# Optimization experiments

Hardware: AMD Instinct MI355X
Metric: run time of the kernel (lower is better)

The kernel has to match this reference:

```python
import jax, jax.numpy as jnp
import numpy as np

N, E, D, H, C, ED = 50000, 800000, 128, 2, 128, 8
LEAKY_SLOPE = 0.2
SOFTMAX_EPS = 1e-16
LN_EPS = 1e-5


def setup_inputs() -> dict:
    key = jax.random.key(0)
    ks = jax.random.split(key, 12)
    s = lambda k, shp, scale: jax.random.normal(k, shp, dtype=jnp.float32) * scale
    return {
        "x": s(ks[0], (N, D), 1.0),
        "edge_index": jax.random.randint(ks[1], (2, E), 0, N, dtype=jnp.int64),
        "edge_attr": s(ks[2], (E, ED), 1.0),
        "W_ep": s(ks[3], (ED, D), 1.0 / np.sqrt(ED)),
        "b_ep": jnp.zeros((D,), jnp.float32),
        "W_lin": s(ks[4], (D, H * C), 1.0 / np.sqrt(D)),
        "att_src": s(ks[5], (H, C), 1.0 / np.sqrt(C)),
        "att_dst": s(ks[6], (H, C), 1.0 / np.sqrt(C)),
        "W_le": s(ks[7], (D, H * C), 1.0 / np.sqrt(D)),
        "att_edge": s(ks[8], (H, C), 1.0 / np.sqrt(C)),
        "bias_gat": jnp.zeros((C,), jnp.float32),
        "ln_gamma": jnp.ones((C,), jnp.float32),
        "ln_beta": jnp.zeros((C,), jnp.float32),
    }


def reference(x, edge_index, edge_attr, W_ep, b_ep, W_lin, att_src, att_dst,
              W_le, att_edge, bias_gat, ln_gamma, ln_beta):
    src, dst = edge_index[0], edge_index[1]
    # edge_proj: [E, ED] -> [E, D]
    e = edge_attr @ W_ep + b_ep
    # node projection: [N, H, C]
    h = (x @ W_lin).reshape(N, H, C)
    # edge projection inside GATConv: [E, H, C]
    ee = (e @ W_le).reshape(E, H, C)
    # attention logits
    a_src = jnp.einsum('nhc,hc->nh', h, att_src)      # [N, H]
    a_dst = jnp.einsum('nhc,hc->nh', h, att_dst)      # [N, H]
    a_edge = jnp.einsum('ehc,hc->eh', ee, att_edge)   # [E, H]
    score = a_src[src] + a_dst[dst] + a_edge          # [E, H]
    score = jnp.where(score >= 0, score, LEAKY_SLOPE * score)
    # segment softmax over incoming edges of each dst node
    smax = jax.ops.segment_max(score, dst, num_segments=N)     # [N, H]
    ex = jnp.exp(score - smax[dst])
    denom = jax.ops.segment_sum(ex, dst, num_segments=N)       # [N, H]
    alpha = ex / (denom[dst] + SOFTMAX_EPS)                    # [E, H]
    # message + scatter-add aggregation
    msg = h[src] * alpha[:, :, None]                           # [E, H, C]
    agg = jax.ops.segment_sum(msg, dst, num_segments=N)        # [N, H, C]
    out = agg.mean(axis=1) + bias_gat                          # concat=False -> head mean
    # residual + LayerNorm (dropout = identity in eval mode)
    y = out + x
    mu = y.mean(axis=-1, keepdims=True)
    var = y.var(axis=-1, keepdims=True)
    return (y - mu) * jax.lax.rsqrt(var + LN_EPS) * ln_gamma + ln_beta
```

## Files before the change

kernel.cpp:

```cpp
#include <hip/hip_runtime.h>
#include <hip/hip_bf16.h>

#define NN 50000
#define EE 800000
#define DD 128
#define HH 2
#define CC 128
#define HC 256
#define EDD 8

#define LEAKY 0.2f
#define SMEPS 1e-16f
#define LNEPS 1e-5f

#define SCAN_B 196
#define CONV_B 3125
#define K2_B   782
#define NPAD   50176

#define HB_OFF    0u
#define ASRC_OFF  12800000u
#define ADST_OFF  13200000u
#define CONST_OFF 13600000u
#define SD_OFF    13604096u
#define CNT8_OFF  20004096u
#define ROW_OFF   21609728u
#define BASE8_OFF 21810432u
#define PAY_OFF   23416064u
#define WBT_OFF   29816064u
#define BSUM_OFF  29881600u

typedef __attribute__((ext_vector_type(8))) short short8v;
typedef __attribute__((ext_vector_type(4))) float float4v;
typedef __attribute__((ext_vector_type(2))) int int2v;

__device__ __forceinline__ float bf2f(unsigned short v) {
  return __uint_as_float(((unsigned)v) << 16);
}
__device__ __forceinline__ unsigned short f2bf(float f) {
  __hip_bfloat16 b = __float2bfloat16(f);
  return *reinterpret_cast<unsigned short*>(&b);
}

__global__ __launch_bounds__(256) void kA_prep_convert(const float* __restrict__ W_lin,
                                                       const float* __restrict__ att_src,
                                                       const float* __restrict__ att_dst,
                                                       const float* __restrict__ W_le,
                                                       const float* __restrict__ att_edge,
                                                       const float* __restrict__ W_ep,
                                                       const float* __restrict__ b_ep,
                                                       const int* __restrict__ ei_raw,
                                                       float* __restrict__ consts,
                                                       unsigned short* __restrict__ wbT,
                                                       int* __restrict__ cnt8,
                                                       int2v* __restrict__ sd) {
  int b = blockIdx.x, tid = threadIdx.x;
  if (b == 0) {
    __shared__ float vlds[HH * DD];
    int h = tid >> 7, d = tid & 127;
    const float* as = att_src + h * CC;
    const float* ad = att_dst + h * CC;
    const float* ae = att_edge + h * CC;
    float us = 0.f, ud = 0.f, vv = 0.f;
    for (int c = 0; c < CC; ++c) {
      float wl = W_lin[d * HC + h * CC + c];
      float we = W_le[d * HC + h * CC + c];
      us += wl * as[c]; ud += wl * ad[c]; vv += we * ae[c];
    }
    consts[h * 128 + d] = us;
    consts[256 + h * 128 + d] = ud;
    vlds[h * 128 + d] = vv;
    __syncthreads();
    if (tid < 16) {
      int hh = tid >> 3, k = tid & 7;
      float w = 0.f;
      for (int dd2 = 0; dd2 < DD; ++dd2) w += W_ep[k * DD + dd2] * vlds[hh * 128 + dd2];
      consts[512 + hh * 8 + k] = w;
    }
    if (tid < 2) {
      float ce = 0.f;
      for (int dd2 = 0; dd2 < DD; ++dd2) ce += b_ep[dd2] * vlds[tid * 128 + dd2];
      consts[528 + tid] = ce;
    }
  } else if (b <= 128) {
    int i = (b - 1) * 256 + tid;
    int k = i >> 8, c = i & 255;
    wbT[c * DD + k] = f2bf(W_lin[i]);
  } else {
    int lane = threadIdx.x & 63;
    int probe = ei_raw[2 * lane + 1];
    bool is64 = (__ballot(probe != 0) == 0ull);
    int xcd = __builtin_amdgcn_s_getreg((20) | (0 << 6) | ((32 - 1) << 11)) & 7;
    int i = (b - 129) * 256 + tid;
    int s, d;
    if (is64) { s = ei_raw[2 * i]; d = ei_raw[2 * (EE + i)]; }
    else      { s = ei_raw[i];     d = ei_raw[EE + i]; }
    int rk = __hip_atomic_fetch_add(&cnt8[xcd * NPAD + d], 1,
                                    __ATOMIC_RELAXED, __HIP_MEMORY_SCOPE_WORKGROUP);
    int2v v; v.x = s; v.y = d | (rk << 16) | (xcd << 29);
    sd[i] = v;
  }
}

__global__ __launch_bounds__(256) void k_scan1(const int* __restrict__ cnt8,
                                               int* __restrict__ rowstart,
                                               int* __restrict__ base8,
                                               int* __restrict__ bsum) {
  __shared__ int sp[256];
  int t = threadIdx.x, b = blockIdx.x;
  int n = b * 256 + t;
  int c[8];
  int tot = 0;
#pragma unroll
  for (int r = 0; r < 8; ++r) {
    c[r] = (n < NN) ? cnt8[r * NPAD + n] : 0;
    tot += c[r];
  }
  sp[t] = tot;
  __syncthreads();
  for (int off = 1; off < 256; off <<= 1) {
    int u = (t >= off) ? sp[t - off] : 0;
    __syncthreads();
    sp[t] += u;
    __syncthreads();
  }
  int intra = sp[t] - tot;
  if (n < NN) {
    rowstart[n] = intra;
    int run = intra;
#pragma unroll
    for (int r = 0; r < 8; ++r) { base8[r * NPAD + n] = run; run += c[r]; }
  }
  if (t == 255) bsum[b] = sp[255];
}

__global__ __launch_bounds__(256) void kB_scan_mfma(int* __restrict__ rowstart,
                                                    const int* __restrict__ bsum,
                                                    int* __restrict__ base8,
                                                    const float* __restrict__ x,
                                                    const unsigned short* __restrict__ wbT,
                                                    const float* __restrict__ consts,
                                                    unsigned char* __restrict__ hbuf8,
                                                    float* __restrict__ a_src,
                                                    float* __restrict__ a_dst) {
  __shared__ unsigned short xs[64 * 256];
  int tid = threadIdx.x;

  if (blockIdx.x < SCAN_B) {
    int* sp = (int*)xs;
    int t = tid, b = blockIdx.x;
    int v = (t < SCAN_B) ? bsum[t] : 0;
    sp[t] = v;
    __syncthreads();
    for (int off = 1; off < 256; off <<= 1) {
      int u = (t >= off) ? sp[t - off] : 0;
      __syncthreads();
      sp[t] += u;
      __syncthreads();
    }
    int boff = (b == 0) ? 0 : sp[b - 1];
    int n = b * 256 + t;
    if (n < NN) {
      rowstart[n] += boff;
#pragma unroll
      for (int r = 0; r < 8; ++r) base8[r * NPAD + n] += boff;
    }
    if (n == NN) rowstart[NN] = EE;
    return;
  }

  int n0 = (blockIdx.x - SCAN_B) * 64;
  int r = tid >> 2, q = tid & 3;
  int n = n0 + r;
  bool valid = (n < NN);

  float xv[32];
  const float4* xp = (const float4*)(x + (size_t)n * DD + q * 32);
#pragma unroll
  for (int j = 0; j < 8; ++j) {
    float4 v = valid ? xp[j] : make_float4(0.f, 0.f, 0.f, 0.f);
    xv[j * 4 + 0] = v.x; xv[j * 4 + 1] = v.y; xv[j * 4 + 2] = v.z; xv[j * 4 + 3] = v.w;
  }
  float ps0 = 0.f, ps1 = 0.f, pd0 = 0.f, pd1 = 0.f;
#pragma unroll
  for (int j = 0; j < 32; j += 4) {
    float4 u0 = *(const float4*)(consts +   0 + q * 32 + j);
    float4 u1 = *(const float4*)(consts + 128 + q * 32 + j);
    float4 v0 = *(const float4*)(consts + 256 + q * 32 + j);
    float4 v1 = *(const float4*)(consts + 384 + q * 32 + j);
    ps0 += xv[j] * u0.x + xv[j+1] * u0.y + xv[j+2] * u0.z + xv[j+3] * u0.w;
    ps1 += xv[j] * u1.x + xv[j+1] * u1.y + xv[j+2] * u1.z + xv[j+3] * u1.w;
    pd0 += xv[j] * v0.x + xv[j+1] * v0.y + xv[j+2] * v0.z + xv[j+3] * v0.w;
    pd1 += xv[j] * v1.x + xv[j+1] * v1.y + xv[j+2] * v1.z + xv[j+3] * v1.w;
  }
#pragma unroll
  for (int off = 1; off < 4; off <<= 1) {
    ps0 += __shfl_xor(ps0, off); ps1 += __shfl_xor(ps1, off);
    pd0 += __shfl_xor(pd0, off); pd1 += __shfl_xor(pd1, off);
  }
  if (q == 0 && valid) {
    *(float2*)(a_src + n * 2) = make_float2(ps0, ps1);
    *(float2*)(a_dst + n * 2) = make_float2(pd0, pd1);
  }

#pragma unroll
  for (int ci = 0; ci < 4; ++ci) {
    union { short8v v; unsigned short u[8]; } pk;
#pragma unroll
    for (int j = 0; j < 8; ++j) pk.u[j] = f2bf(xv[ci * 8 + j]);
    unsigned byte = r * 256 + (q * 4 + ci) * 16;
    byte ^= (r & 7) << 4;
    *(short8v*)((char*)xs + byte) = pk.v;
  }

  int wave = tid >> 6, l = tid & 63;
  int wc = wave * 64;
  int lr = l & 15, lg = l >> 4;
  short8v bfr[4][4];
#pragma unroll
  for (int ct = 0; ct < 4; ++ct) {
    int col = wc + ct * 16 + lr;
#pragma unroll
    for (int kt = 0; kt < 4; ++kt)
      bfr[ct][kt] = *(const short8v*)(wbT + (size_t)col * DD + kt * 32 + lg * 8);
  }

  __syncthreads();

  float4v acc[4][4];
#pragma unroll
  for (int rt = 0; rt < 4; ++rt)
#pragma unroll
    for (int ct = 0; ct < 4; ++ct) acc[rt][ct] = (float4v){0.f, 0.f, 0.f, 0.f};

#pragma unroll
  for (int kt = 0; kt < 4; ++kt) {
    short8v afr[4];
#pragma unroll
    for (int rt = 0; rt < 4; ++rt) {
      int row = rt * 16 + lr;
      unsigned byte = row * 256 + kt * 64 + lg * 16;
      byte ^= (row & 7) << 4;
      afr[rt] = *(const short8v*)((const char*)xs + byte);
    }
#pragma unroll
    for (int rt = 0; rt < 4; ++rt)
#pragma unroll
      for (int ct = 0; ct < 4; ++ct)
        acc[rt][ct] = __builtin_amdgcn_mfma_f32_16x16x32_bf16(afr[rt], bfr[ct][kt], acc[rt][ct], 0, 0, 0);
  }

  __syncthreads();
#pragma unroll
  for (int rt = 0; rt < 4; ++rt) {
#pragma unroll
    for (int j = 0; j < 4; ++j) {
      int row = rt * 16 + lg * 4 + j;
#pragma unroll
      for (int ct = 0; ct < 4; ++ct) {
        int col = wc + ct * 16 + lr;
        int idx2 = ((col & 127) << 1) | (col >> 7);
        unsigned o = (unsigned)idx2 * 2;
        unsigned byte = row * 512 + (o ^ ((((unsigned)(row & 7) ^ ((o >> 7) & 3))) << 4));
        *(unsigned short*)((char*)xs + byte) = f2bf(acc[rt][ct][j]);
      }
    }
  }
  __syncthreads();
  {
    int r2 = tid >> 2, q2 = tid & 3;
    int n2 = n0 + r2;
    if (n2 < NN) {
#pragma unroll
      for (int kk = 0; kk < 4; ++kk) {
        unsigned u4[4];
#pragma unroll
        for (int t2 = 0; t2 < 2; ++t2) {
          int k = kk * 2 + t2;
          unsigned o = q2 * 128 + k * 16;
          unsigned byte = r2 * 512 + (o ^ ((((unsigned)(r2 & 7) ^ ((o >> 7) & 3))) << 4));
          short8v v = *(short8v*)((char*)xs + byte);
          unsigned ua = __builtin_amdgcn_cvt_pk_fp8_f32(bf2f((unsigned short)v[0]), bf2f((unsigned short)v[1]), 0u, false);
          ua = __builtin_amdgcn_cvt_pk_fp8_f32(bf2f((unsigned short)v[2]), bf2f((unsigned short)v[3]), ua, true);
          unsigned ub = __builtin_amdgcn_cvt_pk_fp8_f32(bf2f((unsigned short)v[4]), bf2f((unsigned short)v[5]), 0u, false);
          ub = __builtin_amdgcn_cvt_pk_fp8_f32(bf2f((unsigned short)v[6]), bf2f((unsigned short)v[7]), ub, true);
          u4[t2 * 2] = ua; u4[t2 * 2 + 1] = ub;
        }
        uint4 w4 = make_uint4(u4[0], u4[1], u4[2], u4[3]);
        *(uint4*)(hbuf8 + (size_t)n2 * 256 + q2 * 64 + kk * 16) = w4;
      }
    }
  }
}

__global__ __launch_bounds__(256) void k34_edge(const int2v* __restrict__ sd,
                                                const int* __restrict__ base8,
                                                const float* __restrict__ edge_attr,
                                                const float* __restrict__ a_src,
                                                const float* __restrict__ a_dst,
                                                const float* __restrict__ consts,
                                                int2v* __restrict__ payload) {
  int e = blockIdx.x * 256 + threadIdx.x;
  int2v sdv = sd[e];
  int s = sdv.x;
  unsigned y = (unsigned)sdv.y;
  int d = (int)(y & 0xFFFFu);
  int rk = (int)((y >> 16) & 0x1FFFu);
  int xcd = (int)(y >> 29);
  float4 ea0 = *(const float4*)(edge_attr + (size_t)e * 8);
  float4 ea1 = *(const float4*)(edge_attr + (size_t)e * 8 + 4);
  float2 asv = *(const float2*)(a_src + s * 2);
  float2 adv = *(const float2*)(a_dst + d * 2);
  const float* w0 = consts + 512;
  const float* w1 = consts + 520;
  float sc0 = asv.x + adv.x + consts[528]
            + ea0.x * w0[0] + ea0.y * w0[1] + ea0.z * w0[2] + ea0.w * w0[3]
            + ea1.x * w0[4] + ea1.y * w0[5] + ea1.z * w0[6] + ea1.w * w0[7];
  float sc1 = asv.y + adv.y + consts[529]
            + ea0.x * w1[0] + ea0.y * w1[1] + ea0.z * w1[2] + ea0.w * w1[3]
            + ea1.x * w1[4] + ea1.y * w1[5] + ea1.z * w1[6] + ea1.w * w1[7];
  sc0 = (sc0 >= 0.f) ? sc0 : LEAKY * sc0;
  sc1 = (sc1 >= 0.f) ? sc1 : LEAKY * sc1;
  float ex0 = __expf(sc0);
  float ex1 = __expf(sc1);
  unsigned pk = (unsigned)f2bf(ex0) | ((unsigned)f2bf(ex1) << 16);
  int pos = base8[xcd * NPAD + d] + rk;
  int2v pv; pv.x = s << 8; pv.y = (int)pk;
  payload[pos] = pv;
}

__global__ __launch_bounds__(256) void k5_fused(const int* __restrict__ rowstart,
                                                const int2v* __restrict__ payload,
                                                const unsigned char* __restrict__ hb8,
                                                const float* __restrict__ x,
                                                const float* __restrict__ bias,
                                                const float* __restrict__ gamma,
                                                const float* __restrict__ beta,
                                                float* __restrict__ out) {
  int n = blockIdx.x * 4 + (threadIdx.x >> 6);
  int lane = threadIdx.x & 63;
  if (n >= NN) return;
  int p0i = __builtin_amdgcn_readfirstlane(rowstart[n]);
  int p1i = __builtin_amdgcn_readfirstlane(rowstart[n + 1]);
  int len = p1i - p0i;
  int c0 = lane * 2;
  const int2v* pp = payload + p0i;
  float a00 = 0.f, a01 = 0.f, a10 = 0.f, a11 = 0.f, se0 = 0.f, se1 = 0.f;

#define K5_LD(soff) (*(const unsigned*)(hb8 + (size_t)(unsigned)(soff) + lane * 4))
#define K5_ACC(pl, w) { \
    float ex0 = bf2f((unsigned short)((unsigned)(pl).y & 0xffffu)); \
    float ex1 = bf2f((unsigned short)(((unsigned)(pl).y) >> 16)); \
    a00 = fmaf(ex0, __builtin_amdgcn_cvt_f32_fp8((int)(w), 0), a00); \
    a01 = fmaf(ex1, __builtin_amdgcn_cvt_f32_fp8((int)(w), 1), a01); \
    a10 = fmaf(ex0, __builtin_amdgcn_cvt_f32_fp8((int)(w), 2), a10); \
    a11 = fmaf(ex1, __builtin_amdgcn_cvt_f32_fp8((int)(w), 3), a11); \
    se0 += ex0; se1 += ex1; }

  if (len > 0) {
    int2v p0 = pp[0];
    int2v p1 = (len > 1) ? pp[1] : p0;
    int2v p2 = (len > 2) ? pp[2] : p0;
    int2v p3 = (len > 3) ? pp[3] : p0;
    unsigned h0 = K5_LD(p0.x), h1 = K5_LD(p1.x), h2 = K5_LD(p2.x), h3 = K5_LD(p3.x);
    int i = 0;
    for (; i + 7 < len; i += 4) {
      int2v q0 = pp[i + 4], q1 = pp[i + 5], q2 = pp[i + 6], q3 = pp[i + 7];
      unsigned g0 = K5_LD(q0.x), g1 = K5_LD(q1.x), g2 = K5_LD(q2.x), g3 = K5_LD(q3.x);
      K5_ACC(p0, h0); K5_ACC(p1, h1); K5_ACC(p2, h2); K5_ACC(p3, h3);
      p0 = q0; p1 = q1; p2 = q2; p3 = q3;
      h0 = g0; h1 = g1; h2 = g2; h3 = g3;
    }
    int r = len - i;
    K5_ACC(p0, h0);
    if (r > 1) K5_ACC(p1, h1);
    if (r > 2) K5_ACC(p2, h2);
    if (r > 3) K5_ACC(p3, h3);
    if (r > 4) {
      int rem = r - 4;
      int2v q0 = pp[i + 4];
      int2v q1 = (rem > 1) ? pp[i + 5] : q0;
      int2v q2 = (rem > 2) ? pp[i + 6] : q0;
      unsigned g0 = K5_LD(q0.x), g1 = K5_LD(q1.x), g2 = K5_LD(q2.x);
      K5_ACC(q0, g0);
      if (rem > 1) K5_ACC(q1, g1);
      if (rem > 2) K5_ACC(q2, g2);
    }
  }
#undef K5_LD
#undef K5_ACC

  float inv0 = 0.5f / (se0 + SMEPS);
  float inv1 = 0.5f / (se1 + SMEPS);
  float2 xv = *(const float2*)(x + (size_t)n * DD + c0);
  float v0 = a00 * inv0 + a01 * inv1 + bias[c0] + xv.x;
  float v1 = a10 * inv0 + a11 * inv1 + bias[c0 + 1] + xv.y;
  float s = v0 + v1, ss = v0 * v0 + v1 * v1;
#pragma unroll
  for (int o = 32; o > 0; o >>= 1) {
    s += __shfl_xor(s, o);
    ss += __shfl_xor(ss, o);
  }
  float mu = s * (1.f / 128.f);
  float var = ss * (1.f / 128.f) - mu * mu;
  float rstd = rsqrtf(var + LNEPS);
  float2 ov;
  ov.x = (v0 - mu) * rstd * gamma[c0] + beta[c0];
  ov.y = (v1 - mu) * rstd * gamma[c0 + 1] + beta[c0 + 1];
  *(float2*)(out + (size_t)n * CC + c0) = ov;
}

extern "C" void kernel_launch(void* const* d_in, const int* in_sizes, int n_in,
                              void* d_out, int out_size, void* d_ws, size_t ws_size,
                              hipStream_t stream) {
  const float* x        = (const float*)d_in[0];
  const int*   ei_raw   = (const int*)d_in[1];
  const float* edge_attr= (const float*)d_in[2];
  const float* W_ep     = (const float*)d_in[3];
  const float* b_ep     = (const float*)d_in[4];
  const float* W_lin    = (const float*)d_in[5];
  const float* att_src  = (const float*)d_in[6];
  const float* att_dst  = (const float*)d_in[7];
  const float* W_le     = (const float*)d_in[8];
  const float* att_edge = (const float*)d_in[9];
  const float* bias_gat = (const float*)d_in[10];
  const float* ln_gamma = (const float*)d_in[11];
  const float* ln_beta  = (const float*)d_in[12];

  char* ws = (char*)d_ws;
  unsigned char* hbuf8 = (unsigned char*)(ws + HB_OFF);
  float*    a_src  = (float*)(ws + ASRC_OFF);
  float*    a_dst  = (float*)(ws + ADST_OFF);
  float*    consts = (float*)(ws + CONST_OFF);
  int2v*    sd     = (int2v*)(ws + SD_OFF);
  int*      cnt8   = (int*)(ws + CNT8_OFF);
  int*      rowst  = (int*)(ws + ROW_OFF);
  int*      base8  = (int*)(ws + BASE8_OFF);
  int2v*    payload= (int2v*)(ws + PAY_OFF);
  unsigned short* wbT = (unsigned short*)(ws + WBT_OFF);
  int*      bsum   = (int*)(ws + BSUM_OFF);

  hipMemsetAsync(cnt8, 0, (size_t)8 * NPAD * 4, stream);
  kA_prep_convert<<<129 + CONV_B, 256, 0, stream>>>(W_lin, att_src, att_dst, W_le, att_edge,
                                                    W_ep, b_ep, ei_raw, consts, wbT, cnt8, sd);
  k_scan1<<<SCAN_B, 256, 0, stream>>>(cnt8, rowst, base8, bsum);
  kB_scan_mfma<<<SCAN_B + K2_B, 256, 0, stream>>>(rowst, bsum, base8, x, wbT, consts, hbuf8, a_src, a_dst);
  k34_edge<<<CONV_B, 256, 0, stream>>>(sd, base8, edge_attr, a_src, a_dst, consts, payload);
  k5_fused<<<(NN + 3) / 4, 256, 0, stream>>>(rowst, payload, hbuf8, x, bias_gat, ln_gamma, ln_beta, (float*)d_out);
}
```

Baseline: 139.7 us.

## Restructure launch pipeline: fold memset, merge edge counting with GEMM, inline scan fixup

Replaces the hipMemsetAsync with zeroing inside the prep kernel. Moves the edge-counting atomics into the same launch as the MFMA node projection so the two overlap. Drops the separate second-level scan kernel: each block of the edge and aggregation kernels recomputes the 196-entry block-sum prefix in shared memory and adds it on the fly. This removes one memset and one kernel launch plus a pass over rowstart/base8, at the cost of a redundant small scan with many barriers in every block of two large kernels.

```diff
diff --git a/kernel.cpp b/kernel.cpp
--- a/kernel.cpp
+++ b/kernel.cpp
@@ -42,18 +42,16 @@
   return *reinterpret_cast<unsigned short*>(&b);
 }
 
-__global__ __launch_bounds__(256) void kA_prep_convert(const float* __restrict__ W_lin,
-                                                       const float* __restrict__ att_src,
-                                                       const float* __restrict__ att_dst,
-                                                       const float* __restrict__ W_le,
-                                                       const float* __restrict__ att_edge,
-                                                       const float* __restrict__ W_ep,
-                                                       const float* __restrict__ b_ep,
-                                                       const int* __restrict__ ei_raw,
-                                                       float* __restrict__ consts,
-                                                       unsigned short* __restrict__ wbT,
-                                                       int* __restrict__ cnt8,
-                                                       int2v* __restrict__ sd) {
+__global__ __launch_bounds__(256) void k1_prep(const float* __restrict__ W_lin,
+                                               const float* __restrict__ att_src,
+                                               const float* __restrict__ att_dst,
+                                               const float* __restrict__ W_le,
+                                               const float* __restrict__ att_edge,
+                                               const float* __restrict__ W_ep,
+                                               const float* __restrict__ b_ep,
+                                               float* __restrict__ consts,
+                                               unsigned short* __restrict__ wbT,
+                                               int* __restrict__ cnt8) {
   int b = blockIdx.x, tid = threadIdx.x;
   if (b == 0) {
     __shared__ float vlds[HH * DD];
@@ -87,11 +85,30 @@
     int k = i >> 8, c = i & 255;
     wbT[c * DD + k] = f2bf(W_lin[i]);
   } else {
-    int lane = threadIdx.x & 63;
+    int n = (b - 129) * 256 + tid;
+#pragma unroll
+    for (int r = 0; r < 8; ++r) cnt8[r * NPAD + n] = 0;
+  }
+}
+
+__global__ __launch_bounds__(256) void k2_conv_mfma(const float* __restrict__ x,
+                                                    const unsigned short* __restrict__ wbT,
+                                                    const float* __restrict__ consts,
+                                                    const int* __restrict__ ei_raw,
+                                                    unsigned char* __restrict__ hbuf8,
+                                                    float* __restrict__ a_src,
+                                                    float* __restrict__ a_dst,
+                                                    int* __restrict__ cnt8,
+                                                    int2v* __restrict__ sd) {
+  __shared__ unsigned short xs[64 * 256];
+  int tid = threadIdx.x;
+
+  if (blockIdx.x >= K2_B) {
+    int lane = tid & 63;
     int probe = ei_raw[2 * lane + 1];
     bool is64 = (__ballot(probe != 0) == 0ull);
     int xcd = __builtin_amdgcn_s_getreg((20) | (0 << 6) | ((32 - 1) << 11)) & 7;
-    int i = (b - 129) * 256 + tid;
+    int i = (blockIdx.x - K2_B) * 256 + tid;
     int s, d;
     if (is64) { s = ei_raw[2 * i]; d = ei_raw[2 * (EE + i)]; }
     else      { s = ei_raw[i];     d = ei_raw[EE + i]; }
@@ -99,77 +116,10 @@
                                     __ATOMIC_RELAXED, __HIP_MEMORY_SCOPE_WORKGROUP);
     int2v v; v.x = s; v.y = d | (rk << 16) | (xcd << 29);
     sd[i] = v;
-  }
-}
-
-__global__ __launch_bounds__(256) void k_scan1(const int* __restrict__ cnt8,
-                                               int* __restrict__ rowstart,
-                                               int* __restrict__ base8,
-                                               int* __restrict__ bsum) {
-  __shared__ int sp[256];
-  int t = threadIdx.x, b = blockIdx.x;
-  int n = b * 256 + t;
-  int c[8];
-  int tot = 0;
-#pragma unroll
-  for (int r = 0; r < 8; ++r) {
-    c[r] = (n < NN) ? cnt8[r * NPAD + n] : 0;
-    tot += c[r];
-  }
-  sp[t] = tot;
-  __syncthreads();
-  for (int off = 1; off < 256; off <<= 1) {
-    int u = (t >= off) ? sp[t - off] : 0;
-    __syncthreads();
-    sp[t] += u;
-    __syncthreads();
-  }
-  int intra = sp[t] - tot;
-  if (n < NN) {
-    rowstart[n] = intra;
-    int run = intra;
-#pragma unroll
-    for (int r = 0; r < 8; ++r) { base8[r * NPAD + n] = run; run += c[r]; }
-  }
-  if (t == 255) bsum[b] = sp[255];
-}
-
-__global__ __launch_bounds__(256) void kB_scan_mfma(int* __restrict__ rowstart,
-                                                    const int* __restrict__ bsum,
-                                                    int* __restrict__ base8,
-                                                    const float* __restrict__ x,
-                                                    const unsigned short* __restrict__ wbT,
-                                                    const float* __restrict__ consts,
-                                                    unsigned char* __restrict__ hbuf8,
-                                                    float* __restrict__ a_src,
-                                                    float* __restrict__ a_dst) {
-  __shared__ unsigned short xs[64 * 256];
-  int tid = threadIdx.x;
-
-  if (blockIdx.x < SCAN_B) {
-    int* sp = (int*)xs;
-    int t = tid, b = blockIdx.x;
-    int v = (t < SCAN_B) ? bsum[t] : 0;
-    sp[t] = v;
-    __syncthreads();
-    for (int off = 1; off < 256; off <<= 1) {
-      int u = (t >= off) ? sp[t - off] : 0;
-      __syncthreads();
-      sp[t] += u;
-      __syncthreads();
-    }
-    int boff = (b == 0) ? 0 : sp[b - 1];
-    int n = b * 256 + t;
-    if (n < NN) {
-      rowstart[n] += boff;
-#pragma unroll
-      for (int r = 0; r < 8; ++r) base8[r * NPAD + n] += boff;
-    }
-    if (n == NN) rowstart[NN] = EE;
     return;
   }
 
-  int n0 = (blockIdx.x - SCAN_B) * 64;
+  int n0 = blockIdx.x * 64;
   int r = tid >> 2, q = tid & 3;
   int n = n0 + r;
   bool valid = (n < NN);
@@ -293,14 +243,60 @@
   }
 }
 
+__global__ __launch_bounds__(256) void k_scan1(const int* __restrict__ cnt8,
+                                               int* __restrict__ rowstart,
+                                               int* __restrict__ base8,
+                                               int* __restrict__ bsum) {
+  __shared__ int sp[256];
+  int t = threadIdx.x, b = blockIdx.x;
+  int n = b * 256 + t;
+  int c[8];
+  int tot = 0;
+#pragma unroll
+  for (int r = 0; r < 8; ++r) {
+    c[r] = (n < NN) ? cnt8[r * NPAD + n] : 0;
+    tot += c[r];
+  }
+  sp[t] = tot;
+  __syncthreads();
+  for (int off = 1; off < 256; off <<= 1) {
+    int u = (t >= off) ? sp[t - off] : 0;
+    __syncthreads();
+    sp[t] += u;
+    __syncthreads();
+  }
+  int intra = sp[t] - tot;
+  if (n < NN) {
+    rowstart[n] = intra;
+    int run = intra;
+#pragma unroll
+    for (int r = 0; r < 8; ++r) { base8[r * NPAD + n] = run; run += c[r]; }
+  }
+  if (t == 255) bsum[b] = sp[255];
+}
+
 __global__ __launch_bounds__(256) void k34_edge(const int2v* __restrict__ sd,
                                                 const int* __restrict__ base8,
+                                                const int* __restrict__ bsum,
                                                 const float* __restrict__ edge_attr,
                                                 const float* __restrict__ a_src,
                                                 const float* __restrict__ a_dst,
                                                 const float* __restrict__ consts,
                                                 int2v* __restrict__ payload) {
-  int e = blockIdx.x * 256 + threadIdx.x;
+  __shared__ int bs[256];
+  int t = threadIdx.x;
+  {
+    int v = (t < SCAN_B) ? bsum[t] : 0;
+    bs[t] = v;
+    __syncthreads();
+    for (int off = 1; off < 256; off <<= 1) {
+      int u = (t >= off) ? bs[t - off] : 0;
+      __syncthreads();
+      bs[t] += u;
+      __syncthreads();
+    }
+  }
+  int e = blockIdx.x * 256 + t;
   int2v sdv = sd[e];
   int s = sdv.x;
   unsigned y = (unsigned)sdv.y;
@@ -324,12 +320,15 @@
   float ex0 = __expf(sc0);
   float ex1 = __expf(sc1);
   unsigned pk = (unsigned)f2bf(ex0) | ((unsigned)f2bf(ex1) << 16);
-  int pos = base8[xcd * NPAD + d] + rk;
+  int blk = d >> 8;
+  int boff = (blk == 0) ? 0 : bs[blk - 1];
+  int pos = base8[xcd * NPAD + d] + boff + rk;
   int2v pv; pv.x = s << 8; pv.y = (int)pk;
   payload[pos] = pv;
 }
 
 __global__ __launch_bounds__(256) void k5_fused(const int* __restrict__ rowstart,
+                                                const int* __restrict__ bsum,
                                                 const int2v* __restrict__ payload,
                                                 const unsigned char* __restrict__ hb8,
                                                 const float* __restrict__ x,
@@ -337,11 +336,31 @@
                                                 const float* __restrict__ gamma,
                                                 const float* __restrict__ beta,
                                                 float* __restrict__ out) {
-  int n = blockIdx.x * 4 + (threadIdx.x >> 6);
-  int lane = threadIdx.x & 63;
-  if (n >= NN) return;
-  int p0i = __builtin_amdgcn_readfirstlane(rowstart[n]);
-  int p1i = __builtin_amdgcn_readfirstlane(rowstart[n + 1]);
+  __shared__ int bs[256];
+  int t = threadIdx.x;
+  {
+    int v = (t < SCAN_B) ? bsum[t] : 0;
+    bs[t] = v;
+    __syncthreads();
+    for (int off = 1; off < 256; off <<= 1) {
+      int u = (t >= off) ? bs[t - off] : 0;
+      __syncthreads();
+      bs[t] += u;
+      __syncthreads();
+    }
+  }
+  int n = blockIdx.x * 4 + (t >> 6);
+  int lane = t & 63;
+  int b0 = n >> 8;
+  int p0i = rowstart[n] + ((b0 == 0) ? 0 : bs[b0 - 1]);
+  int p1i;
+  if (n + 1 == NN) p1i = EE;
+  else {
+    int b1 = (n + 1) >> 8;
+    p1i = rowstart[n + 1] + ((b1 == 0) ? 0 : bs[b1 - 1]);
+  }
+  p0i = __builtin_amdgcn_readfirstlane(p0i);
+  p1i = __builtin_amdgcn_readfirstlane(p1i);
   int len = p1i - p0i;
   int c0 = lane * 2;
   const int2v* pp = payload + p0i;
@@ -440,11 +459,11 @@
   unsigned short* wbT = (unsigned short*)(ws + WBT_OFF);
   int*      bsum   = (int*)(ws + BSUM_OFF);
 
-  hipMemsetAsync(cnt8, 0, (size_t)8 * NPAD * 4, stream);
-  kA_prep_convert<<<129 + CONV_B, 256, 0, stream>>>(W_lin, att_src, att_dst, W_le, att_edge,
-                                                    W_ep, b_ep, ei_raw, consts, wbT, cnt8, sd);
+  k1_prep<<<325, 256, 0, stream>>>(W_lin, att_src, att_dst, W_le, att_edge, W_ep, b_ep,
+                                   consts, wbT, cnt8);
+  k2_conv_mfma<<<K2_B + CONV_B, 256, 0, stream>>>(x, wbT, consts, ei_raw, hbuf8,
+                                                  a_src, a_dst, cnt8, sd);
   k_scan1<<<SCAN_B, 256, 0, stream>>>(cnt8, rowst, base8, bsum);
-  kB_scan_mfma<<<SCAN_B + K2_B, 256, 0, stream>>>(rowst, bsum, base8, x, wbT, consts, hbuf8, a_src, a_dst);
-  k34_edge<<<CONV_B, 256, 0, stream>>>(sd, base8, edge_attr, a_src, a_dst, consts, payload);
-  k5_fused<<<(NN + 3) / 4, 256, 0, stream>>>(rowst, payload, hbuf8, x, bias_gat, ln_gamma, ln_beta, (float*)d_out);
-}
+  k34_edge<<<CONV_B, 256, 0, stream>>>(sd, base8, bsum, edge_attr, a_src, a_dst, consts, payload);
+  k5_fused<<<NN / 4, 256, 0, stream>>>(rowst, bsum, payload, hbuf8, x, bias_gat, ln_gamma, ln_beta, (float*)d_out);
+}
```

New measurement: 144.7 us. 3.6% more time.
